# Performance work log

Measured on AMD Instinct MI355X. Metric: run time of the kernel, lower is better.

The kernel has to match this reference:

```python
import jax, jax.numpy as jnp
import numpy as np

B, S, I, O = 64, 512, 256, 256


def setup_inputs() -> dict:
    key = jax.random.key(0)
    ks = jax.random.split(key, 7)
    s_i = 1.0 / np.sqrt(I)
    s_o = 1.0 / np.sqrt(O)
    return {
        "x": jax.random.normal(ks[0], (B, S, I), dtype=jnp.float32),
        "h0": jax.random.normal(ks[1], (B, O), dtype=jnp.float32) * 0.1,
        "c0": jax.random.normal(ks[2], (B, O), dtype=jnp.float32) * 0.1,
        # gate order: [f, i, g, o]; Linear convention y = x @ W.T + b
        "Wh": jax.random.normal(ks[3], (4, O, O), dtype=jnp.float32) * s_o,
        "bh": jax.random.normal(ks[4], (4, O), dtype=jnp.float32) * s_o,
        "Wx": jax.random.normal(ks[5], (4, O, I), dtype=jnp.float32) * s_i,
        "bx": jax.random.normal(ks[6], (4, O), dtype=jnp.float32) * s_i,
    }


def reference(x, h0, c0, Wh, bh, Wx, bx):
    # Precompute all input-side gate projections in one big GEMM: [S, B, 4, O]
    xg = jnp.einsum('bsi,goi->sbgo', x, Wx) + bx + bh  # fold both biases here

    def step(carry, xt):
        h, c = carry
        g = jnp.einsum('bo,gpo->bgp', h, Wh) + xt  # [B, 4, O]
        f = jax.nn.sigmoid(g[:, 0])
        i = jax.nn.sigmoid(g[:, 1])
        gt = jnp.tanh(g[:, 2])
        o = jax.nn.sigmoid(g[:, 3])
        c = c * f + i * gt
        h = o * jnp.tanh(c)
        return (h, c), h

    (hT, cT), hs = jax.lax.scan(step, (h0, c0), xg)
    h_seq = jnp.transpose(hs, (1, 0, 2))  # [B, S, O]
    return h_seq, hT, cT
```

## Files before the change

kernel.cpp:

```cpp
#include <hip/hip_runtime.h>


#define SS 512

typedef _Float16 h2 __attribute__((ext_vector_type(2)));

__device__ __forceinline__ h2 bch(unsigned u) { return __builtin_bit_cast(h2, u); }

#if __has_builtin(__builtin_amdgcn_fdot2)
__device__ __forceinline__ float dot2f(h2 a, h2 b, float c) {
  return __builtin_amdgcn_fdot2(a, b, c, false);
}
#else
__device__ __forceinline__ float dot2f(h2 a, h2 b, float c) {
  return c + (float)a[0] * (float)b[0] + (float)a[1] * (float)b[1];
}
#endif

__device__ __forceinline__ float sigm(float x) { return 1.f / (1.f + __expf(-x)); }
__device__ __forceinline__ float tanh_f(float x) {
  float e = __expf(-2.f * fabsf(x));
  float r = (1.f - e) / (1.f + e);
  return copysignf(r, x);
}

__global__ __launch_bounds__(256) void xg_gemm(
    const float* __restrict__ X, const float* __restrict__ W,
    const float* __restrict__ bx, const float* __restrict__ bh,
    float* __restrict__ out)
{
  __shared__ float As[64][68];
  __shared__ float Bs[64][68];
  const int bm = blockIdx.x >> 4;
  const int bn = blockIdx.x & 15;
  const int tid = threadIdx.x;
  const int tn = tid & 15, tm = tid >> 4;
  const int row0 = bm * 64, col0 = bn * 64;
  float acc[4][4] = {};

  for (int k0 = 0; k0 < 256; k0 += 64) {
#pragma unroll
    for (int i = 0; i < 4; i++) {
      const int m = (tid >> 4) + i * 16;
      const int k = (tid & 15) * 4;
      float4 av = *(const float4*)&X[(size_t)(row0 + m) * 256 + k0 + k];
      *(float4*)&As[m][k] = av;
      float4 wv = *(const float4*)&W[(size_t)(col0 + m) * 256 + k0 + k];
      Bs[k + 0][m] = wv.x; Bs[k + 1][m] = wv.y;
      Bs[k + 2][m] = wv.z; Bs[k + 3][m] = wv.w;
    }
    __syncthreads();
#pragma unroll 8
    for (int kk = 0; kk < 64; kk++) {
      const float a0 = As[tm * 4 + 0][kk];
      const float a1 = As[tm * 4 + 1][kk];
      const float a2 = As[tm * 4 + 2][kk];
      const float a3 = As[tm * 4 + 3][kk];
      const float4 bv = *(const float4*)&Bs[kk][tn * 4];
      acc[0][0] = fmaf(a0, bv.x, acc[0][0]); acc[0][1] = fmaf(a0, bv.y, acc[0][1]);
      acc[0][2] = fmaf(a0, bv.z, acc[0][2]); acc[0][3] = fmaf(a0, bv.w, acc[0][3]);
      acc[1][0] = fmaf(a1, bv.x, acc[1][0]); acc[1][1] = fmaf(a1, bv.y, acc[1][1]);
      acc[1][2] = fmaf(a1, bv.z, acc[1][2]); acc[1][3] = fmaf(a1, bv.w, acc[1][3]);
      acc[2][0] = fmaf(a2, bv.x, acc[2][0]); acc[2][1] = fmaf(a2, bv.y, acc[2][1]);
      acc[2][2] = fmaf(a2, bv.z, acc[2][2]); acc[2][3] = fmaf(a2, bv.w, acc[2][3]);
      acc[3][0] = fmaf(a3, bv.x, acc[3][0]); acc[3][1] = fmaf(a3, bv.y, acc[3][1]);
      acc[3][2] = fmaf(a3, bv.z, acc[3][2]); acc[3][3] = fmaf(a3, bv.w, acc[3][3]);
    }
    __syncthreads();
  }

  float bias[4];
#pragma unroll
  for (int j = 0; j < 4; j++) {
    const int col = col0 + tn * 4 + j;
    bias[j] = bx[col] + bh[col];
  }
#pragma unroll
  for (int i = 0; i < 4; i++) {
    float4 o4;
    o4.x = acc[i][0] + bias[0]; o4.y = acc[i][1] + bias[1];
    o4.z = acc[i][2] + bias[2]; o4.w = acc[i][3] + bias[3];
    *(float4*)&out[(size_t)(row0 + tm * 4 + i) * 1024 + col0 + tn * 4] = o4;
  }
}

__global__ __launch_bounds__(512, 2) void lstm_scan2(
    const float* __restrict__ xg,
    const float* __restrict__ Wh,
    const float* __restrict__ h0,
    const float* __restrict__ c0,
    float* __restrict__ out)
{
  __shared__ __align__(16) _Float16 wl[2 * 8 * 512 * 8];
  __shared__ __align__(16) _Float16 h_sh[256];
  __shared__ float io_i[256];
  __shared__ float io_o[256];

  const int tid = threadIdx.x;
  const int b = blockIdx.x;

  const float* r0 = Wh + (size_t)tid * 256;
  const float* r1 = Wh + (size_t)(tid + 512) * 256;

  h2 w0[96], w1[96];
#pragma unroll
  for (int j = 0; j < 96; ++j) {
    float2 a = *(const float2*)&r0[2 * j];
    float2 c = *(const float2*)&r1[2 * j];
    h2 wa; wa[0] = (_Float16)a.x; wa[1] = (_Float16)a.y; w0[j] = wa;
    h2 wc; wc[0] = (_Float16)c.x; wc[1] = (_Float16)c.y; w1[j] = wc;
  }
#pragma unroll
  for (int c = 0; c < 8; ++c) {
#pragma unroll
    for (int e = 0; e < 8; ++e) {
      wl[((size_t)(c)*512 + tid) * 8 + e]     = (_Float16)r0[192 + c * 8 + e];
      wl[((size_t)(8 + c)*512 + tid) * 8 + e] = (_Float16)r1[192 + c * 8 + e];
    }
  }
  if (tid < 256) h_sh[tid] = (_Float16)h0[(size_t)b * 256 + tid];
  float cr = (tid < 256) ? c0[(size_t)b * 256 + tid] : 0.f;
  __syncthreads();

  const float* xr = xg + (size_t)b * SS * 1024;
  float* hs = out + (size_t)b * SS * 256;

  for (int t = 0; t < SS; ++t) {
    const float xg0 = xr[(size_t)t * 1024 + tid];
    const float xg1 = xr[(size_t)t * 1024 + tid + 512];

    float A0 = 0.f, B0 = 0.f, A1 = 0.f, B1 = 0.f;
#pragma unroll
    for (int c2 = 0; c2 < 12; ++c2) {
      uint4 ha = *(const uint4*)&h_sh[c2 * 16];
      uint4 hb = *(const uint4*)&h_sh[c2 * 16 + 8];
      const int j = c2 * 8;
      A0 = dot2f(w0[j + 0], bch(ha.x), A0); A1 = dot2f(w1[j + 0], bch(ha.x), A1);
      B0 = dot2f(w0[j + 1], bch(ha.y), B0); B1 = dot2f(w1[j + 1], bch(ha.y), B1);
      A0 = dot2f(w0[j + 2], bch(ha.z), A0); A1 = dot2f(w1[j + 2], bch(ha.z), A1);
      B0 = dot2f(w0[j + 3], bch(ha.w), B0); B1 = dot2f(w1[j + 3], bch(ha.w), B1);
      A0 = dot2f(w0[j + 4], bch(hb.x), A0); A1 = dot2f(w1[j + 4], bch(hb.x), A1);
      B0 = dot2f(w0[j + 5], bch(hb.y), B0); B1 = dot2f(w1[j + 5], bch(hb.y), B1);
      A0 = dot2f(w0[j + 6], bch(hb.z), A0); A1 = dot2f(w1[j + 6], bch(hb.z), A1);
      B0 = dot2f(w0[j + 7], bch(hb.w), B0); B1 = dot2f(w1[j + 7], bch(hb.w), B1);
    }
#pragma unroll
    for (int c = 0; c < 8; ++c) {
      uint4 hw = *(const uint4*)&h_sh[192 + c * 8];
      uint4 wa = *(const uint4*)&wl[((size_t)(c)*512 + tid) * 8];
      uint4 wb = *(const uint4*)&wl[((size_t)(8 + c)*512 + tid) * 8];
      A0 = dot2f(bch(wa.x), bch(hw.x), A0); A1 = dot2f(bch(wb.x), bch(hw.x), A1);
      B0 = dot2f(bch(wa.y), bch(hw.y), B0); B1 = dot2f(bch(wb.y), bch(hw.y), B1);
      A0 = dot2f(bch(wa.z), bch(hw.z), A0); A1 = dot2f(bch(wb.z), bch(hw.z), A1);
      B0 = dot2f(bch(wa.w), bch(hw.w), B0); B1 = dot2f(bch(wb.w), bch(hw.w), B1);
    }
    const float y0 = A0 + B0 + xg0;
    const float y1 = A1 + B1 + xg1;

    float u0 = 0.f, u1 = 0.f;
    if (tid < 256) {
      u0 = sigm(y0);
      u1 = tanh_f(y1);
    } else {
      io_i[tid - 256] = sigm(y0);
      io_o[tid - 256] = sigm(y1);
    }
    __syncthreads();

    if (tid < 256) {
      cr = cr * u0 + io_i[tid] * u1;
      const float h = io_o[tid] * tanh_f(cr);
      hs[(size_t)t * 256 + tid] = h;
      h_sh[tid] = (_Float16)h;
      if (t == SS - 1) {
        out[8388608 + (size_t)b * 256 + tid] = h;
        out[8404992 + (size_t)b * 256 + tid] = cr;
      }
    }
    __syncthreads();
  }
}

extern "C" void kernel_launch(void* const* d_in, const int* in_sizes, int n_in,
                              void* d_out, int out_size, void* d_ws, size_t ws_size,
                              hipStream_t stream) {
  const float* x  = (const float*)d_in[0];
  const float* h0 = (const float*)d_in[1];
  const float* c0 = (const float*)d_in[2];
  const float* Wh = (const float*)d_in[3];
  const float* bh = (const float*)d_in[4];
  const float* Wx = (const float*)d_in[5];
  const float* bx = (const float*)d_in[6];
  float* out = (float*)d_out;

  float* xg = (float*)d_ws;

  xg_gemm<<<dim3(8192), dim3(256), 0, stream>>>(x, Wx, bx, bh, xg);
  lstm_scan2<<<dim3(64), dim3(512), 0, stream>>>(xg, Wh, h0, c0, out);
}
```

Before: 1.262 ms.

## Restructure LSTM scan with split-K packed fp16 FMA and DPP reductions

Rewrites the recurrent scan kernel so that each group of 8 threads covers 4 hidden units across all 4 gates, with each thread handling a 32-wide K slice. Products are accumulated with packed half-precision FMA and then reduced across lanes using DPP adds. The hidden state is double-buffered in padded shared memory, which cuts the per-step barriers from two to one and removes the io_i/io_o exchange. Accumulating in fp16 and only widening at the end risks extra precision loss compared with the fdot2 fp32 accumulation it replaces.

Result: slower. 1.737 ms (+37.6%).

```diff
diff --git a/kernel.cpp b/kernel.cpp
--- a/kernel.cpp
+++ b/kernel.cpp
@@ -16,6 +16,24 @@
   return c + (float)a[0] * (float)b[0] + (float)a[1] * (float)b[1];
 }
 #endif
+
+__device__ __forceinline__ h2 pkfma(h2 a, h2 b, h2 c) {
+  return __builtin_elementwise_fma(a, b, c);
+}
+
+template <int CTRL>
+__device__ __forceinline__ float dppadd(float x) {
+  int s = __builtin_bit_cast(int, x);
+  int v = __builtin_amdgcn_update_dpp(0, s, CTRL, 0xF, 0xF, true);
+  return x + __builtin_bit_cast(float, v);
+}
+
+__device__ __forceinline__ float xor4add(float x) {
+  int s = __builtin_bit_cast(int, x);
+  int v = __builtin_amdgcn_update_dpp(0, s, 0x12C, 0xF, 0x5, false);
+  v = __builtin_amdgcn_update_dpp(v, s, 0x124, 0xF, 0xA, false);
+  return x + __builtin_bit_cast(float, v);
+}
 
 __device__ __forceinline__ float sigm(float x) { return 1.f / (1.f + __expf(-x)); }
 __device__ __forceinline__ float tanh_f(float x) {
@@ -84,97 +102,119 @@
   }
 }
 
-__global__ __launch_bounds__(512, 2) void lstm_scan2(
+__global__ __launch_bounds__(512, 2) void lstm_scan6(
     const float* __restrict__ xg,
     const float* __restrict__ Wh,
     const float* __restrict__ h0,
     const float* __restrict__ c0,
     float* __restrict__ out)
 {
-  __shared__ __align__(16) _Float16 wl[2 * 8 * 512 * 8];
-  __shared__ __align__(16) _Float16 h_sh[256];
-  __shared__ float io_i[256];
-  __shared__ float io_o[256];
-
-  const int tid = threadIdx.x;
+  __shared__ __align__(16) _Float16 wl[4 * 4 * 512 * 8];
+  __shared__ __align__(16) _Float16 h_sh[2][8 * 40];
+
+  const int t = threadIdx.x;
   const int b = blockIdx.x;
-
-  const float* r0 = Wh + (size_t)tid * 256;
-  const float* r1 = Wh + (size_t)(tid + 512) * 256;
-
-  h2 w0[96], w1[96];
-#pragma unroll
-  for (int j = 0; j < 96; ++j) {
-    float2 a = *(const float2*)&r0[2 * j];
-    float2 c = *(const float2*)&r1[2 * j];
-    h2 wa; wa[0] = (_Float16)a.x; wa[1] = (_Float16)a.y; w0[j] = wa;
-    h2 wc; wc[0] = (_Float16)c.x; wc[1] = (_Float16)c.y; w1[j] = wc;
-  }
-#pragma unroll
-  for (int c = 0; c < 8; ++c) {
-#pragma unroll
-    for (int e = 0; e < 8; ++e) {
-      wl[((size_t)(c)*512 + tid) * 8 + e]     = (_Float16)r0[192 + c * 8 + e];
-      wl[((size_t)(8 + c)*512 + tid) * 8 + e] = (_Float16)r1[192 + c * 8 + e];
-    }
-  }
-  if (tid < 256) h_sh[tid] = (_Float16)h0[(size_t)b * 256 + tid];
-  float cr = (tid < 256) ? c0[(size_t)b * 256 + tid] : 0.f;
+  const int rg = t >> 3;
+  const int q  = t & 7;
+  const int e  = q & 3;
+  const bool owner = (q < 4);
+  const int m  = 4 * rg + e;
+  const int kb = 32 * q;
+
+  h2 wv[12][16];
+#pragma unroll
+  for (int r = 0; r < 12; ++r) {
+    const float* row = Wh + (size_t)((r >> 2) * 256 + 4 * rg + (r & 3)) * 256 + kb;
+#pragma unroll
+    for (int j = 0; j < 16; ++j) {
+      float2 a = *(const float2*)&row[2 * j];
+      h2 x; x[0] = (_Float16)a.x; x[1] = (_Float16)a.y;
+      wv[r][j] = x;
+    }
+  }
+#pragma unroll
+  for (int rp = 0; rp < 4; ++rp) {
+    const float* row = Wh + (size_t)(768 + 4 * rg + rp) * 256 + kb;
+#pragma unroll
+    for (int j4 = 0; j4 < 4; ++j4) {
+      const int hb = ((rp * 4 + j4) * 512 + t) * 8;
+#pragma unroll
+      for (int d = 0; d < 4; ++d) {
+        float2 a = *(const float2*)&row[8 * j4 + 2 * d];
+        wl[hb + 2 * d + 0] = (_Float16)a.x;
+        wl[hb + 2 * d + 1] = (_Float16)a.y;
+      }
+    }
+  }
+  if (t < 256) h_sh[0][(t >> 5) * 40 + (t & 31)] = (_Float16)h0[(size_t)b * 256 + t];
+  float cr = owner ? c0[(size_t)b * 256 + m] : 0.f;
   __syncthreads();
 
   const float* xr = xg + (size_t)b * SS * 1024;
   float* hs = out + (size_t)b * SS * 256;
-
-  for (int t = 0; t < SS; ++t) {
-    const float xg0 = xr[(size_t)t * 1024 + tid];
-    const float xg1 = xr[(size_t)t * 1024 + tid + 512];
-
-    float A0 = 0.f, B0 = 0.f, A1 = 0.f, B1 = 0.f;
-#pragma unroll
-    for (int c2 = 0; c2 < 12; ++c2) {
-      uint4 ha = *(const uint4*)&h_sh[c2 * 16];
-      uint4 hb = *(const uint4*)&h_sh[c2 * 16 + 8];
-      const int j = c2 * 8;
-      A0 = dot2f(w0[j + 0], bch(ha.x), A0); A1 = dot2f(w1[j + 0], bch(ha.x), A1);
-      B0 = dot2f(w0[j + 1], bch(ha.y), B0); B1 = dot2f(w1[j + 1], bch(ha.y), B1);
-      A0 = dot2f(w0[j + 2], bch(ha.z), A0); A1 = dot2f(w1[j + 2], bch(ha.z), A1);
-      B0 = dot2f(w0[j + 3], bch(ha.w), B0); B1 = dot2f(w1[j + 3], bch(ha.w), B1);
-      A0 = dot2f(w0[j + 4], bch(hb.x), A0); A1 = dot2f(w1[j + 4], bch(hb.x), A1);
-      B0 = dot2f(w0[j + 5], bch(hb.y), B0); B1 = dot2f(w1[j + 5], bch(hb.y), B1);
-      A0 = dot2f(w0[j + 6], bch(hb.z), A0); A1 = dot2f(w1[j + 6], bch(hb.z), A1);
-      B0 = dot2f(w0[j + 7], bch(hb.w), B0); B1 = dot2f(w1[j + 7], bch(hb.w), B1);
-    }
-#pragma unroll
-    for (int c = 0; c < 8; ++c) {
-      uint4 hw = *(const uint4*)&h_sh[192 + c * 8];
-      uint4 wa = *(const uint4*)&wl[((size_t)(c)*512 + tid) * 8];
-      uint4 wb = *(const uint4*)&wl[((size_t)(8 + c)*512 + tid) * 8];
-      A0 = dot2f(bch(wa.x), bch(hw.x), A0); A1 = dot2f(bch(wb.x), bch(hw.x), A1);
-      B0 = dot2f(bch(wa.y), bch(hw.y), B0); B1 = dot2f(bch(wb.y), bch(hw.y), B1);
-      A0 = dot2f(bch(wa.z), bch(hw.z), A0); A1 = dot2f(bch(wb.z), bch(hw.z), A1);
-      B0 = dot2f(bch(wa.w), bch(hw.w), B0); B1 = dot2f(bch(wb.w), bch(hw.w), B1);
-    }
-    const float y0 = A0 + B0 + xg0;
-    const float y1 = A1 + B1 + xg1;
-
-    float u0 = 0.f, u1 = 0.f;
-    if (tid < 256) {
-      u0 = sigm(y0);
-      u1 = tanh_f(y1);
-    } else {
-      io_i[tid - 256] = sigm(y0);
-      io_o[tid - 256] = sigm(y1);
-    }
-    __syncthreads();
-
-    if (tid < 256) {
-      cr = cr * u0 + io_i[tid] * u1;
-      const float h = io_o[tid] * tanh_f(cr);
-      hs[(size_t)t * 256 + tid] = h;
-      h_sh[tid] = (_Float16)h;
-      if (t == SS - 1) {
-        out[8388608 + (size_t)b * 256 + tid] = h;
-        out[8404992 + (size_t)b * 256 + tid] = cr;
+  h2 kOne; kOne[0] = (_Float16)1.0f; kOne[1] = (_Float16)1.0f;
+
+  for (int s = 0; s < SS; ++s) {
+    const int p = s & 1;
+    float x_f = 0.f, x_i = 0.f, x_g = 0.f, x_o = 0.f;
+    if (owner) {
+      const float* xp = xr + (size_t)s * 1024 + m;
+      x_f = xp[0]; x_i = xp[256]; x_g = xp[512]; x_o = xp[768];
+    }
+
+    h2 acc[16] = {};
+#pragma unroll
+    for (int i = 0; i < 4; ++i) {
+      const uint4 hw = *(const uint4*)&h_sh[p][q * 40 + i * 8];
+#pragma unroll
+      for (int r = 0; r < 12; ++r) {
+        acc[r] = pkfma(wv[r][4 * i + 0], bch(hw.x), acc[r]);
+        acc[r] = pkfma(wv[r][4 * i + 1], bch(hw.y), acc[r]);
+        acc[r] = pkfma(wv[r][4 * i + 2], bch(hw.z), acc[r]);
+        acc[r] = pkfma(wv[r][4 * i + 3], bch(hw.w), acc[r]);
+      }
+#pragma unroll
+      for (int rp = 0; rp < 4; ++rp) {
+        const uint4 wq = *(const uint4*)&wl[((rp * 4 + i) * 512 + t) * 8];
+        acc[12 + rp] = pkfma(bch(wq.x), bch(hw.x), acc[12 + rp]);
+        acc[12 + rp] = pkfma(bch(wq.y), bch(hw.y), acc[12 + rp]);
+        acc[12 + rp] = pkfma(bch(wq.z), bch(hw.z), acc[12 + rp]);
+        acc[12 + rp] = pkfma(bch(wq.w), bch(hw.w), acc[12 + rp]);
+      }
+    }
+
+    float y[16];
+#pragma unroll
+    for (int r = 0; r < 16; ++r) y[r] = dot2f(acc[r], kOne, 0.f);
+#pragma unroll
+    for (int r = 0; r < 16; ++r) y[r] = dppadd<0xB1>(y[r]);
+#pragma unroll
+    for (int r = 0; r < 16; ++r) y[r] = dppadd<0x4E>(y[r]);
+#pragma unroll
+    for (int r = 0; r < 16; ++r) y[r] = xor4add(y[r]);
+
+    float yg[4];
+#pragma unroll
+    for (int g4 = 0; g4 < 4; ++g4) {
+      float z = y[4 * g4 + 0];
+      z = (e == 1) ? y[4 * g4 + 1] : z;
+      z = (e == 2) ? y[4 * g4 + 2] : z;
+      z = (e == 3) ? y[4 * g4 + 3] : z;
+      yg[g4] = z;
+    }
+
+    if (owner) {
+      const float f  = sigm(yg[0] + x_f);
+      const float ii = sigm(yg[1] + x_i);
+      const float gg = tanh_f(yg[2] + x_g);
+      const float oo = sigm(yg[3] + x_o);
+      cr = cr * f + ii * gg;
+      const float h = oo * tanh_f(cr);
+      hs[(size_t)s * 256 + m] = h;
+      h_sh[p ^ 1][(m >> 5) * 40 + (m & 31)] = (_Float16)h;
+      if (s == SS - 1) {
+        out[8388608 + (size_t)b * 256 + m] = h;
+        out[8404992 + (size_t)b * 256 + m] = cr;
       }
     }
     __syncthreads();
@@ -196,5 +236,5 @@
   float* xg = (float*)d_ws;
 
   xg_gemm<<<dim3(8192), dim3(256), 0, stream>>>(x, Wx, bx, bh, xg);
-  lstm_scan2<<<dim3(64), dim3(512), 0, stream>>>(xg, Wh, h0, c0, out);
-}
+  lstm_scan6<<<dim3(64), dim3(512), 0, stream>>>(xg, Wh, h0, c0, out);
+}
```
